# Kernel tuning notes

Measured on AMD Instinct MI355X. Metric: run time of the kernel, lower is better.

The kernel has to match this reference:

```python
import jax, jax.numpy as jnp
import numpy as np

NUM_HEADS = 16
EPS = 1e-12  # softmax_2relu eps
MASK_VALUE = -1e9  # stands in for torch.finfo(dtype).min; relu zeroes it anyway


def setup_inputs() -> dict:
    key = jax.random.key(0)
    k1, k2, k3 = jax.random.split(key, 3)
    B, S, D = 4, 1024, 1024
    hidden_states = jax.random.normal(k1, (B, S, D), dtype=jnp.float32)
    c_attn_w = jax.random.normal(k2, (D, 3 * D), dtype=jnp.float32) * 0.02
    c_attn_b = jnp.zeros((3 * D,), dtype=jnp.float32)
    c_proj_w = jax.random.normal(k3, (D, D), dtype=jnp.float32) * 0.02
    c_proj_b = jnp.zeros((D,), dtype=jnp.float32)
    return {
        "hidden_states": hidden_states,
        "c_attn_w": c_attn_w,
        "c_attn_b": c_attn_b,
        "c_proj_w": c_proj_w,
        "c_proj_b": c_proj_b,
    }


def softmax_2relu(scores, axis=-1, eps=EPS):
    r = jax.nn.relu(scores)
    n = scores.shape[axis]
    return (r + eps / n) / (jnp.sum(r, axis=axis, keepdims=True) + eps)


def reference(hidden_states, c_attn_w, c_attn_b, c_proj_w, c_proj_b):
    B, S, D = hidden_states.shape
    H = NUM_HEADS
    dh = D // H

    # fused QKV projection (Conv1D: x @ W + b)
    qkv = hidden_states @ c_attn_w + c_attn_b  # [B, S, 3D]
    q, k, v = jnp.split(qkv, 3, axis=-1)

    def to_heads(t):
        return t.reshape(B, S, H, dh).transpose(0, 2, 1, 3)  # [B, H, S, dh]

    q, k, v = to_heads(q), to_heads(k), to_heads(v)

    # attention scores, scaled
    scores = jnp.einsum("bhqd,bhkd->bhqk", q, k) / jnp.sqrt(
        jnp.asarray(dh, dtype=hidden_states.dtype)
    )

    # causal mask: masked positions set to large negative (relu -> 0)
    causal = jnp.tril(jnp.ones((S, S), dtype=bool))
    scores = jnp.where(causal[None, None, :, :], scores, MASK_VALUE)

    # custom relu-softmax normalization (softmax_2relu)
    attn = softmax_2relu(scores, axis=-1)

    ctx = jnp.einsum("bhqk,bhkd->bhqd", attn, v)  # [B, H, S, dh]
    ctx = ctx.transpose(0, 2, 1, 3).reshape(B, S, D)

    out = ctx @ c_proj_w + c_proj_b
    return out
```

## Files before the change

### kernel.cpp

```cpp
#include <hip/hip_runtime.h>
#include <hip/hip_bf16.h>

typedef unsigned short u16;
typedef unsigned int u32;

#define AS1 __attribute__((address_space(1)))
#define AS3 __attribute__((address_space(3)))

typedef __attribute__((ext_vector_type(8))) __bf16 bf16x8;
typedef __attribute__((ext_vector_type(4))) float f32x4;
typedef __attribute__((ext_vector_type(8))) u16 u16x8;

static __device__ __forceinline__ u16 f2bf(float f) {
    u32 x = __builtin_bit_cast(u32, f);
    u32 r = (x + 0x7fffu + ((x >> 16) & 1u)) >> 16;
    return (u16)r;
}
static __device__ __forceinline__ float bf2f(u16 u) {
    u32 x = ((u32)u) << 16;
    return __builtin_bit_cast(float, x);
}
static __device__ __forceinline__ void gload_lds16(const void* g, void* l) {
    __builtin_amdgcn_global_load_lds((const AS1 u32*)g, (AS3 u32*)l, 16, 0, 0);
}
static __device__ __forceinline__ u32 cvtpk(float lo, float hi) {
    u32 r;
    asm("v_cvt_pk_bf16_f32 %0, %1, %2" : "=v"(r) : "v"(lo), "v"(hi));
    return r;
}

__global__ __launch_bounds__(256) void k_cast_bf16(const float* __restrict__ in,
                                                   u16* __restrict__ out, int n8) {
    int i = blockIdx.x * 256 + threadIdx.x;
    if (i >= n8) return;
    typedef __attribute__((ext_vector_type(4))) float fx4;
    const fx4* p = (const fx4*)in;
    fx4 a = p[2 * i], b = p[2 * i + 1];
    u16x8 o;
    o[0] = f2bf(a[0]); o[1] = f2bf(a[1]); o[2] = f2bf(a[2]); o[3] = f2bf(a[3]);
    o[4] = f2bf(b[0]); o[5] = f2bf(b[1]); o[6] = f2bf(b[2]); o[7] = f2bf(b[3]);
    *(u16x8*)(out + (size_t)i * 8) = o;
}

__global__ __launch_bounds__(256) void k_wtrans(const float* __restrict__ W,
                                                u16* __restrict__ Wt, int K_, int N_) {
    __shared__ u16 T[64][65];
    int nt = blockIdx.x, kt = blockIdx.y;
    int t = threadIdx.x, c = t & 63, r0 = t >> 6;
#pragma unroll
    for (int i = 0; i < 16; i++) {
        int k = r0 + i * 4;
        T[k][c] = f2bf(W[(size_t)(kt * 64 + k) * N_ + nt * 64 + c]);
    }
    __syncthreads();
#pragma unroll
    for (int i = 0; i < 16; i++) {
        int nn = r0 + i * 4;
        Wt[(size_t)(nt * 64 + nn) * K_ + kt * 64 + c] = T[c][nn];
    }
}

template <int EPI>
__global__ __launch_bounds__(256, 2) void k_gemm(
    const u16* __restrict__ A, const u16* __restrict__ Bt,
    const float* __restrict__ bias, float* __restrict__ outf,
    u16* __restrict__ Qb, u16* __restrict__ Kb, u16* __restrict__ Vb,
    int Msz, int Nsz, int Ksz) {
    __shared__ u16 Al[128 * 64];
    __shared__ u16 Bl[128 * 64];
    int tid = threadIdx.x;
    int m0 = blockIdx.x * 128, n0 = blockIdx.y * 128;
    int w = tid >> 6, lane = tid & 63, l15 = lane & 15, lg = lane >> 4;
    int wr = (w >> 1) * 64, wc = (w & 1) * 64;
    f32x4 acc[4][4] = {};

    for (int k0 = 0; k0 < Ksz; k0 += 64) {
#pragma unroll
        for (int i = 0; i < 4; i++) {
            int c = i * 256 + tid;
            gload_lds16(A + (size_t)(m0 + (c >> 3)) * Ksz + k0 + (c & 7) * 8,
                        &Al[(c & ~63) * 8]);
        }
#pragma unroll
        for (int i = 0; i < 4; i++) {
            int c = i * 256 + tid;
            gload_lds16(Bt + (size_t)(n0 + (c >> 3)) * Ksz + k0 + (c & 7) * 8,
                        &Bl[(c & ~63) * 8]);
        }
        __syncthreads();
#pragma unroll
        for (int kk = 0; kk < 2; kk++) {
            bf16x8 af[4], bfr[4];
#pragma unroll
            for (int m = 0; m < 4; m++)
                af[m] = *(const bf16x8*)&Al[(wr + m * 16 + l15) * 64 + kk * 32 + lg * 8];
#pragma unroll
            for (int n = 0; n < 4; n++)
                bfr[n] = *(const bf16x8*)&Bl[(wc + n * 16 + l15) * 64 + kk * 32 + lg * 8];
#pragma unroll
            for (int m = 0; m < 4; m++)
#pragma unroll
                for (int n = 0; n < 4; n++)
                    acc[m][n] = __builtin_amdgcn_mfma_f32_16x16x32_bf16(af[m], bfr[n], acc[m][n], 0, 0, 0);
        }
        __syncthreads();
    }

    if (EPI == 0) {
#pragma unroll
        for (int n = 0; n < 4; n++) {
            int gn = n0 + wc + n * 16 + l15;
            float bv = bias[gn];
#pragma unroll
            for (int m = 0; m < 4; m++) {
                int gmb = m0 + wr + m * 16 + lg * 4;
#pragma unroll
                for (int r = 0; r < 4; r++)
                    outf[(size_t)(gmb + r) * Nsz + gn] = acc[m][n][r] + bv;
            }
        }
    } else {
        u16* T = Al;
        const int TP = 136;
        float bv[4];
#pragma unroll
        for (int n = 0; n < 4; n++) bv[n] = bias[n0 + wc + n * 16 + l15];
        int lrow = tid >> 3;
        int c0 = (tid & 7) << 4;
        int gcol = n0 + c0;
        int which = gcol >> 10, d = gcol & 1023, h = d >> 6, dd = d & 63;
        u16* dstb = which == 0 ? Qb : (which == 1 ? Kb : Vb);

#define EPI_CHUNK(mc)                                                              \
    {                                                                              \
        __syncthreads();                                                           \
        if (((mc) >> 1) == (w >> 1)) {                                             \
            _Pragma("unroll") for (int n = 0; n < 4; n++) {                        \
                _Pragma("unroll") for (int r = 0; r < 4; r++) {                    \
                    int lr = (lg << 2) + r;                                        \
                    T[lr * TP + wc + (n << 4) + l15] =                             \
                        f2bf(acc[2 * ((mc) & 1)][n][r] + bv[n]);                   \
                    T[(16 + lr) * TP + wc + (n << 4) + l15] =                      \
                        f2bf(acc[2 * ((mc) & 1) + 1][n][r] + bv[n]);               \
                }                                                                  \
            }                                                                      \
        }                                                                          \
        __syncthreads();                                                           \
        int gm = m0 + (mc) * 32 + lrow;                                            \
        int b = gm >> 10, s = gm & 1023;                                           \
        u16* dp = dstb + ((size_t)(b * 16 + h) * 1024 + s) * 64 + dd;              \
        const u16* sp = &T[lrow * TP + c0];                                        \
        *(u16x8*)dp = *(const u16x8*)sp;                                           \
        *(u16x8*)(dp + 8) = *(const u16x8*)(sp + 8);                               \
    }

        EPI_CHUNK(0) EPI_CHUNK(1) EPI_CHUNK(2) EPI_CHUNK(3)
#undef EPI_CHUNK
    }
}

__global__ __launch_bounds__(256) void k_vtrans(const u16* __restrict__ Vb,
                                                u16* __restrict__ Vt,
                                                float* __restrict__ vpart) {
    __shared__ u16 T[64][65];
    __shared__ float red[4][64];
    int st = blockIdx.x, bh = blockIdx.y;
    int t = threadIdx.x, c = t & 63, r0 = t >> 6;
    const u16* Vh = Vb + (size_t)bh * 65536;
    u16* Vth = Vt + (size_t)bh * 65536;
    float a = 0.f;
#pragma unroll
    for (int i = 0; i < 16; i++) {
        int s = r0 + i * 4;
        u16 v = Vh[(size_t)(st * 64 + s) * 64 + c];
        T[s][c] = v;
        a += bf2f(v);
    }
    red[r0][c] = a;
    __syncthreads();
#pragma unroll
    for (int i = 0; i < 16; i++) {
        int d = r0 + i * 4;
        Vth[(size_t)d * 1024 + st * 64 + c] = T[c][d];
    }
    if (r0 == 0)
        vpart[((size_t)bh * 16 + st) * 64 + c] =
            red[0][c] + red[1][c] + red[2][c] + red[3][c];
}

__global__ __launch_bounds__(256) void k_vsum2(const float* __restrict__ vpart,
                                               float* __restrict__ vsum) {
    int idx = blockIdx.x * 256 + threadIdx.x;
    int bh = idx >> 6, d = idx & 63;
    const float* p = vpart + (size_t)bh * 1024 + d;
    float s = 0.f;
#pragma unroll
    for (int st = 0; st < 16; st++) s += p[st * 64];
    vsum[idx] = s;
}

__global__ __launch_bounds__(512, 4) void k_attn(const u16* __restrict__ Qb,
                                                 const u16* __restrict__ Kb,
                                                 const u16* __restrict__ Vt,
                                                 const float* __restrict__ vsum,
                                                 u16* __restrict__ ctx) {
    __shared__ u16 Kl[2][4096];
    __shared__ u16 Vl[2][4096];
    __shared__ u16 Pl[8 * 1024];
    __shared__ float rsw[8][16];
    int tid = threadIdx.x, w = tid >> 6, lane = tid & 63, l15 = lane & 15, lg = lane >> 4;
    int p = blockIdx.x;
    int tb = 7 - (p >> 6);
    int bh = p & 63;
    int qb = tb * 128 + w * 16;
    int nkb = 2 * tb + 2;
    int klast = (qb + 15) >> 6;

    const u16* Qh = Qb + (size_t)bh * 65536;
    const u16* Kh = Kb + (size_t)bh * 65536;
    const u16* Vh = Vt + (size_t)bh * 65536;
    u16* Pw = &Pl[w * 1024];
    int swz = (l15 & 7) << 4;
    int q = qb + l15;

    bf16x8 qf[2];
#pragma unroll
    for (int kk = 0; kk < 2; kk++)
        qf[kk] = *(const bf16x8*)(Qh + (size_t)q * 64 + kk * 32 + lg * 8);
    float vs[4];
#pragma unroll
    for (int n = 0; n < 4; n++) vs[n] = vsum[bh * 64 + n * 16 + l15];

    int srow = tid >> 3, schunk = tid & 7;
    int soff = ((schunk * 16) ^ ((srow & 7) << 4)) >> 1;
    u16* kdst = &Kl[0][0] + w * 512;
    u16* vdst = &Vl[0][0] + w * 512;

    f32x4 ctxa[4] = {};
    float rsp = 0.f;
    int cur = 0;

    gload_lds16(Kh + (size_t)srow * 64 + soff, kdst);
    gload_lds16(Vh + (size_t)srow * 1024 + soff, vdst);
    __syncthreads();

    for (int kb = 0; kb < nkb; kb++) {
        if (kb + 1 < nkb) {
            int nx = cur ^ 1;
            gload_lds16(Kh + (size_t)(((kb + 1) << 6) + srow) * 64 + soff,
                        &Kl[nx][0] + w * 512);
            gload_lds16(Vh + (size_t)srow * 1024 + ((kb + 1) << 6) + soff,
                        &Vl[nx][0] + w * 512);
        }
        if (kb <= klast) {
            bool masked = (kb == klast);
            const char* Kc = (const char*)&Kl[cur][0];
            const char* Vc = (const char*)&Vl[cur][0];
            f32x4 sc[4] = {};
#pragma unroll
            for (int kk = 0; kk < 2; kk++)
#pragma unroll
                for (int n = 0; n < 4; n++) {
                    bf16x8 kf = *(const bf16x8*)(Kc + ((((n * 16 + l15) << 7) + (kk << 6) + (lg << 4)) ^ swz));
                    sc[n] = __builtin_amdgcn_mfma_f32_16x16x32_bf16(kf, qf[kk], sc[n], 0, 0, 0);
                }
            int qml = q - (kb << 6) - (lg << 2);
#pragma unroll
            for (int n = 0; n < 4; n++) {
                float v0 = fmaxf(sc[n][0] * 0.125f, 0.f);
                float v1 = fmaxf(sc[n][1] * 0.125f, 0.f);
                float v2 = fmaxf(sc[n][2] * 0.125f, 0.f);
                float v3 = fmaxf(sc[n][3] * 0.125f, 0.f);
                if (masked) {
                    int c = qml - n * 16;
                    v0 = (0 <= c) ? v0 : 0.f;
                    v1 = (1 <= c) ? v1 : 0.f;
                    v2 = (2 <= c) ? v2 : 0.f;
                    v3 = (3 <= c) ? v3 : 0.f;
                }
                rsp += (v0 + v1) + (v2 + v3);
                u32 w0 = cvtpk(v0, v1), w1 = cvtpk(v2, v3);
                int base = l15 * 128 + n * 32 + lg * 8;
                *(u32*)((char*)Pw + ((base) ^ swz)) = w0;
                *(u32*)((char*)Pw + ((base + 4) ^ swz)) = w1;
            }
            bf16x8 pf0 = *(const bf16x8*)((char*)Pw + ((l15 * 128 + lg * 16) ^ swz));
            bf16x8 pf1 = *(const bf16x8*)((char*)Pw + ((l15 * 128 + 64 + lg * 16) ^ swz));
#pragma unroll
            for (int n = 0; n < 4; n++) {
                bf16x8 vf = *(const bf16x8*)(Vc + ((((n * 16 + l15) << 7) + (lg << 4)) ^ swz));
                ctxa[n] = __builtin_amdgcn_mfma_f32_16x16x32_bf16(pf0, vf, ctxa[n], 0, 0, 0);
            }
#pragma unroll
            for (int n = 0; n < 4; n++) {
                bf16x8 vf = *(const bf16x8*)(Vc + ((((n * 16 + l15) << 7) + 64 + (lg << 4)) ^ swz));
                ctxa[n] = __builtin_amdgcn_mfma_f32_16x16x32_bf16(pf1, vf, ctxa[n], 0, 0, 0);
            }
        }
        __syncthreads();
        cur ^= 1;
    }

    float tsum = rsp;
    tsum += __shfl_xor(tsum, 16);
    tsum += __shfl_xor(tsum, 32);
    rsw[w][l15] = tsum;
    f32x4 rv = *(f32x4*)&rsw[w][lg * 4];
    const float EPS = 1e-12f, EPSN = 1e-12f / 1024.f;
    float inv[4];
#pragma unroll
    for (int r = 0; r < 4; r++) inv[r] = 1.f / (rv[r] + EPS);
    int b = bh >> 4, h = bh & 15;
#pragma unroll
    for (int n = 0; n < 4; n++) {
#pragma unroll
        for (int r = 0; r < 4; r++) {
            int qq = qb + lg * 4 + r;
            float val = (ctxa[n][r] + EPSN * vs[n]) * inv[r];
            ctx[(size_t)(b * 1024 + qq) * 1024 + h * 64 + n * 16 + l15] = f2bf(val);
        }
    }
}

__global__ __launch_bounds__(256) void k_qkfix(const float* __restrict__ X,
                                               const float* __restrict__ W,
                                               const float* __restrict__ bias,
                                               float* __restrict__ Qf,
                                               float* __restrict__ Kf) {
    __shared__ float red[4][8][64];
    int cb = blockIdx.x;
    int b = blockIdx.y >> 1, rh = blockIdx.y & 1;
    int tid = threadIdx.x, w = tid >> 6, lane = tid & 63;
    int col = cb * 64 + lane;

    const float* Wp = W + (size_t)(w * 256) * 3072 + col;
    const float* Xp = X + ((size_t)b * 1024 + rh * 8) * 1024 + w * 256;
    float acc[8] = {};
#pragma unroll 8
    for (int it = 0; it < 256; ++it) {
        float wv = Wp[(size_t)it * 3072];
#pragma unroll
        for (int j = 0; j < 8; j++) acc[j] += Xp[(size_t)j * 1024 + it] * wv;
    }
#pragma unroll
    for (int j = 0; j < 8; j++) red[w][j][lane] = acc[j];
    __syncthreads();

    int isK = cb >> 4, h = cb & 15;
    float* dst = isK ? Kf : Qf;
#pragma unroll
    for (int o = tid; o < 512; o += 256) {
        int j = o >> 6, c = o & 63;
        float s = red[0][j][c] + red[1][j][c] + red[2][j][c] + red[3][j][c];
        dst[((size_t)(b * 16 + h) * 16 + rh * 8 + j) * 64 + c] = s + bias[cb * 64 + c];
    }
}

__global__ __launch_bounds__(256) void k_attnfix(const float* __restrict__ Qf,
                                                 const float* __restrict__ Kf,
                                                 const u16* __restrict__ Vb,
                                                 const float* __restrict__ vsum,
                                                 u16* __restrict__ ctx) {
    __shared__ float ps[16][17];
    __shared__ float dens[16];
    int bh = blockIdx.x, t = threadIdx.x;
    int q = t >> 4, k = t & 15;
    const float* Qr = Qf + ((size_t)bh * 16 + q) * 64;
    const float* Kr = Kf + ((size_t)bh * 16 + k) * 64;
    float s = 0.f;
    for (int d = 0; d < 64; d++) s += Qr[d] * Kr[d];
    s *= 0.125f;
    float p = (k <= q) ? fmaxf(s, 0.f) : 0.f;
    float den = p;
    den += __shfl_xor(den, 1); den += __shfl_xor(den, 2);
    den += __shfl_xor(den, 4); den += __shfl_xor(den, 8);
    ps[q][k] = p;
    if (k == 0) dens[q] = den;
    __syncthreads();
    int d0 = (t & 15) * 4;
    float c[4] = {};
    for (int kk = 0; kk <= q; kk++) {
        float pv = ps[q][kk];
        const u16* vr = Vb + ((size_t)bh * 1024 + kk) * 64 + d0;
        c[0] += pv * bf2f(vr[0]); c[1] += pv * bf2f(vr[1]);
        c[2] += pv * bf2f(vr[2]); c[3] += pv * bf2f(vr[3]);
    }
    float inv = 1.f / (dens[q] + 1e-12f);
    const float EPSN = 1e-12f / 1024.f;
    const float* vs = vsum + bh * 64 + d0;
    int b = bh >> 4, h = bh & 15;
    u16* dst = ctx + (size_t)(b * 1024 + q) * 1024 + h * 64 + d0;
#pragma unroll
    for (int j = 0; j < 4; j++) dst[j] = f2bf((c[j] + EPSN * vs[j]) * inv);
}

extern "C" void kernel_launch(void* const* d_in, const int* in_sizes, int n_in,
                              void* d_out, int out_size, void* d_ws, size_t ws_size,
                              hipStream_t stream) {
    const float* X = (const float*)d_in[0];
    const float* Wqkv = (const float*)d_in[1];
    const float* bqkv = (const float*)d_in[2];
    const float* Wproj = (const float*)d_in[3];
    const float* bproj = (const float*)d_in[4];
    float* out = (float*)d_out;
    char* ws = (char*)d_ws;

    u16* Xb     = (u16*)(ws);
    u16* Wqkvt  = (u16*)(ws + 8388608);
    u16* Wprojt = (u16*)(ws + 14680064);
    u16* Qb     = (u16*)(ws + 16777216);
    u16* Kb     = (u16*)(ws + 25165824);
    u16* Vb     = (u16*)(ws + 33554432);
    u16* Vt     = (u16*)(ws + 41943040);
    float* vsum = (float*)(ws + 50331648);
    float* Qf   = (float*)(ws + 50348032);
    float* Kf   = (float*)(ws + 50610176);
    float* vpart= (float*)(ws + 50872320);
    u16* ctx    = Xb;

    k_cast_bf16<<<dim3(2048), dim3(256), 0, stream>>>(X, Xb, 524288);
    k_wtrans<<<dim3(48, 16), dim3(256), 0, stream>>>(Wqkv, Wqkvt, 1024, 3072);
    k_wtrans<<<dim3(16, 16), dim3(256), 0, stream>>>(Wproj, Wprojt, 1024, 1024);
    k_gemm<1><<<dim3(32, 24), dim3(256), 0, stream>>>(Xb, Wqkvt, bqkv, nullptr,
                                                      Qb, Kb, Vb, 4096, 3072, 1024);
    k_vtrans<<<dim3(16, 64), dim3(256), 0, stream>>>(Vb, Vt, vpart);
    k_vsum2<<<dim3(16), dim3(256), 0, stream>>>(vpart, vsum);
    k_qkfix<<<dim3(32, 8), dim3(256), 0, stream>>>(X, Wqkv, bqkv, Qf, Kf);
    k_attn<<<dim3(512), dim3(512), 0, stream>>>(Qb, Kb, Vt, vsum, ctx);
    k_attnfix<<<dim3(64), dim3(256), 0, stream>>>(Qf, Kf, Vb, vsum, ctx);
    k_gemm<0><<<dim3(32, 8), dim3(256), 0, stream>>>(ctx, Wprojt, bproj, out,
                                                     nullptr, nullptr, nullptr, 4096, 1024, 1024);
}
```

Baseline: 138.5 us.

## Fuse prep kernels, fold V transpose into QKV epilogue, retile projection GEMM

Merges the X cast and both weight transposes into one k_prep launch. The QKV GEMM epilogue now writes V directly in transposed layout and emits per-tile V column sums, which removes the separate k_vtrans pass. It still writes only the first 32 rows of V per head in row-major form, presumably for k_attnfix. The output projection moves to a dedicated 128x64-tile GEMM that launches twice as many blocks, and s_setprio hints are added around the MFMA sections of the attention kernel. The tradeoffs are fewer launches and one less global V round trip, against more complex epilogue LDS access patterns and strided Vt writes.

```diff
diff --git a/kernel.cpp b/kernel.cpp
--- a/kernel.cpp
+++ b/kernel.cpp
@@ -29,24 +29,34 @@
     return r;
 }
 
-__global__ __launch_bounds__(256) void k_cast_bf16(const float* __restrict__ in,
-                                                   u16* __restrict__ out, int n8) {
-    int i = blockIdx.x * 256 + threadIdx.x;
-    if (i >= n8) return;
-    typedef __attribute__((ext_vector_type(4))) float fx4;
-    const fx4* p = (const fx4*)in;
-    fx4 a = p[2 * i], b = p[2 * i + 1];
-    u16x8 o;
-    o[0] = f2bf(a[0]); o[1] = f2bf(a[1]); o[2] = f2bf(a[2]); o[3] = f2bf(a[3]);
-    o[4] = f2bf(b[0]); o[5] = f2bf(b[1]); o[6] = f2bf(b[2]); o[7] = f2bf(b[3]);
-    *(u16x8*)(out + (size_t)i * 8) = o;
-}
-
-__global__ __launch_bounds__(256) void k_wtrans(const float* __restrict__ W,
-                                                u16* __restrict__ Wt, int K_, int N_) {
+__global__ __launch_bounds__(256) void k_prep(const float* __restrict__ X,
+                                              u16* __restrict__ Xb,
+                                              const float* __restrict__ Wqkv,
+                                              u16* __restrict__ Wqkvt,
+                                              const float* __restrict__ Wproj,
+                                              u16* __restrict__ Wprojt) {
     __shared__ u16 T[64][65];
-    int nt = blockIdx.x, kt = blockIdx.y;
-    int t = threadIdx.x, c = t & 63, r0 = t >> 6;
+    int bid = blockIdx.x, t = threadIdx.x;
+    if (bid < 2048) {
+        int i = bid * 256 + t;
+        typedef __attribute__((ext_vector_type(4))) float fx4;
+        const fx4* p = (const fx4*)X;
+        fx4 a = p[2 * i], b = p[2 * i + 1];
+        u16x8 o;
+        o[0] = f2bf(a[0]); o[1] = f2bf(a[1]); o[2] = f2bf(a[2]); o[3] = f2bf(a[3]);
+        o[4] = f2bf(b[0]); o[5] = f2bf(b[1]); o[6] = f2bf(b[2]); o[7] = f2bf(b[3]);
+        *(u16x8*)(Xb + (size_t)i * 8) = o;
+        return;
+    }
+    const float* W; u16* Wt; int N_, nt, kt;
+    if (bid < 2816) {
+        W = Wqkv; Wt = Wqkvt; N_ = 3072;
+        int u = bid - 2048; nt = u % 48; kt = u / 48;
+    } else {
+        W = Wproj; Wt = Wprojt; N_ = 1024;
+        int u = bid - 2816; nt = u & 15; kt = u >> 4;
+    }
+    int c = t & 63, r0 = t >> 6;
 #pragma unroll
     for (int i = 0; i < 16; i++) {
         int k = r0 + i * 4;
@@ -56,7 +66,7 @@
 #pragma unroll
     for (int i = 0; i < 16; i++) {
         int nn = r0 + i * 4;
-        Wt[(size_t)(nt * 64 + nn) * K_ + kt * 64 + c] = T[c][nn];
+        Wt[(size_t)(nt * 64 + nn) * 1024 + kt * 64 + c] = T[c][nn];
     }
 }
 
@@ -65,6 +75,7 @@
     const u16* __restrict__ A, const u16* __restrict__ Bt,
     const float* __restrict__ bias, float* __restrict__ outf,
     u16* __restrict__ Qb, u16* __restrict__ Kb, u16* __restrict__ Vb,
+    u16* __restrict__ Vt, float* __restrict__ vpart,
     int Msz, int Nsz, int Ksz) {
     __shared__ u16 Al[128 * 64];
     __shared__ u16 Bl[128 * 64];
@@ -130,6 +141,11 @@
         int gcol = n0 + c0;
         int which = gcol >> 10, d = gcol & 1023, h = d >> 6, dd = d & 63;
         u16* dstb = which == 0 ? Qb : (which == 1 ? Kb : Vb);
+        bool isV = (n0 >= 2048);
+        int s0 = m0 & 1023, bq = m0 >> 10;
+        int dl = tid >> 1, sh = tid & 1;
+        int bhV = bq * 16 + ((n0 - 2048) >> 6) + (dl >> 6);
+        float vp0 = 0.f, vp1 = 0.f;
 
 #define EPI_CHUNK(mc)                                                              \
     {                                                                              \
@@ -146,46 +162,104 @@
             }                                                                      \
         }                                                                          \
         __syncthreads();                                                           \
-        int gm = m0 + (mc) * 32 + lrow;                                            \
-        int b = gm >> 10, s = gm & 1023;                                           \
-        u16* dp = dstb + ((size_t)(b * 16 + h) * 1024 + s) * 64 + dd;              \
-        const u16* sp = &T[lrow * TP + c0];                                        \
-        *(u16x8*)dp = *(const u16x8*)sp;                                           \
-        *(u16x8*)(dp + 8) = *(const u16x8*)(sp + 8);                               \
+        if (!isV) {                                                                \
+            int gm = m0 + (mc) * 32 + lrow;                                        \
+            int b = gm >> 10, s = gm & 1023;                                       \
+            u16* dp = dstb + ((size_t)(b * 16 + h) * 1024 + s) * 64 + dd;          \
+            const u16* sp = &T[lrow * TP + c0];                                    \
+            *(u16x8*)dp = *(const u16x8*)sp;                                       \
+            *(u16x8*)(dp + 8) = *(const u16x8*)(sp + 8);                           \
+        } else {                                                                   \
+            if ((mc) == 0 && s0 == 0) {                                            \
+                u16* dp = dstb + ((size_t)(bq * 16 + h) * 1024 + lrow) * 64 + dd;  \
+                const u16* sp = &T[lrow * TP + c0];                                \
+                *(u16x8*)dp = *(const u16x8*)sp;                                   \
+                *(u16x8*)(dp + 8) = *(const u16x8*)(sp + 8);                       \
+            }                                                                      \
+            float vls = 0.f;                                                       \
+            u16x8 o0, o1;                                                          \
+            _Pragma("unroll") for (int r = 0; r < 8; r++) {                        \
+                u16 v = T[((sh << 4) + r) * TP + dl];                              \
+                o0[r] = v; vls += bf2f(v);                                         \
+            }                                                                      \
+            _Pragma("unroll") for (int r = 0; r < 8; r++) {                        \
+                u16 v = T[((sh << 4) + 8 + r) * TP + dl];                          \
+                o1[r] = v; vls += bf2f(v);                                         \
+            }                                                                      \
+            vls += __shfl_xor(vls, 1);                                             \
+            if ((mc) < 2) vp0 += vls; else vp1 += vls;                             \
+            u16* vtp = Vt + (size_t)bhV * 65536 + (size_t)(dl & 63) * 1024 +       \
+                       s0 + (mc) * 32 + (sh << 4);                                 \
+            *(u16x8*)vtp = o0;                                                     \
+            *(u16x8*)(vtp + 8) = o1;                                               \
+        }                                                                          \
     }
 
         EPI_CHUNK(0) EPI_CHUNK(1) EPI_CHUNK(2) EPI_CHUNK(3)
 #undef EPI_CHUNK
-    }
-}
-
-__global__ __launch_bounds__(256) void k_vtrans(const u16* __restrict__ Vb,
-                                                u16* __restrict__ Vt,
-                                                float* __restrict__ vpart) {
-    __shared__ u16 T[64][65];
-    __shared__ float red[4][64];
-    int st = blockIdx.x, bh = blockIdx.y;
-    int t = threadIdx.x, c = t & 63, r0 = t >> 6;
-    const u16* Vh = Vb + (size_t)bh * 65536;
-    u16* Vth = Vt + (size_t)bh * 65536;
-    float a = 0.f;
-#pragma unroll
-    for (int i = 0; i < 16; i++) {
-        int s = r0 + i * 4;
-        u16 v = Vh[(size_t)(st * 64 + s) * 64 + c];
-        T[s][c] = v;
-        a += bf2f(v);
-    }
-    red[r0][c] = a;
-    __syncthreads();
-#pragma unroll
-    for (int i = 0; i < 16; i++) {
-        int d = r0 + i * 4;
-        Vth[(size_t)d * 1024 + st * 64 + c] = T[c][d];
-    }
-    if (r0 == 0)
-        vpart[((size_t)bh * 16 + st) * 64 + c] =
-            red[0][c] + red[1][c] + red[2][c] + red[3][c];
+
+        if (isV && sh == 0) {
+            int st0 = s0 >> 6;
+            vpart[((size_t)bhV * 16 + st0) * 64 + (dl & 63)] = vp0;
+            vpart[((size_t)bhV * 16 + st0 + 1) * 64 + (dl & 63)] = vp1;
+        }
+    }
+}
+
+__global__ __launch_bounds__(256, 2) void k_gemmP(
+    const u16* __restrict__ A, const u16* __restrict__ Bt,
+    const float* __restrict__ bias, float* __restrict__ outf) {
+    __shared__ u16 Al[128 * 64];
+    __shared__ u16 Bl[64 * 64];
+    int tid = threadIdx.x;
+    int m0 = blockIdx.x * 128, n0 = blockIdx.y * 64;
+    int w = tid >> 6, lane = tid & 63, l15 = lane & 15, lg = lane >> 4;
+    int wr = (w >> 1) * 64, wc = (w & 1) * 32;
+    f32x4 acc[4][2] = {};
+
+    for (int k0 = 0; k0 < 1024; k0 += 64) {
+#pragma unroll
+        for (int i = 0; i < 4; i++) {
+            int c = i * 256 + tid;
+            gload_lds16(A + (size_t)(m0 + (c >> 3)) * 1024 + k0 + (c & 7) * 8,
+                        &Al[(c & ~63) * 8]);
+        }
+#pragma unroll
+        for (int i = 0; i < 2; i++) {
+            int c = i * 256 + tid;
+            gload_lds16(Bt + (size_t)(n0 + (c >> 3)) * 1024 + k0 + (c & 7) * 8,
+                        &Bl[(c & ~63) * 8]);
+        }
+        __syncthreads();
+#pragma unroll
+        for (int kk = 0; kk < 2; kk++) {
+            bf16x8 af[4], bfr[2];
+#pragma unroll
+            for (int m = 0; m < 4; m++)
+                af[m] = *(const bf16x8*)&Al[(wr + m * 16 + l15) * 64 + kk * 32 + lg * 8];
+#pragma unroll
+            for (int n = 0; n < 2; n++)
+                bfr[n] = *(const bf16x8*)&Bl[(wc + n * 16 + l15) * 64 + kk * 32 + lg * 8];
+#pragma unroll
+            for (int m = 0; m < 4; m++)
+#pragma unroll
+                for (int n = 0; n < 2; n++)
+                    acc[m][n] = __builtin_amdgcn_mfma_f32_16x16x32_bf16(af[m], bfr[n], acc[m][n], 0, 0, 0);
+        }
+        __syncthreads();
+    }
+#pragma unroll
+    for (int n = 0; n < 2; n++) {
+        int gn = n0 + wc + n * 16 + l15;
+        float bv = bias[gn];
+#pragma unroll
+        for (int m = 0; m < 4; m++) {
+            int gmb = m0 + wr + m * 16 + lg * 4;
+#pragma unroll
+            for (int r = 0; r < 4; r++)
+                outf[(size_t)(gmb + r) * 1024 + gn] = acc[m][n][r] + bv;
+        }
+    }
 }
 
 __global__ __launch_bounds__(256) void k_vsum2(const float* __restrict__ vpart,
@@ -257,6 +331,7 @@
             const char* Kc = (const char*)&Kl[cur][0];
             const char* Vc = (const char*)&Vl[cur][0];
             f32x4 sc[4] = {};
+            __builtin_amdgcn_s_setprio(1);
 #pragma unroll
             for (int kk = 0; kk < 2; kk++)
 #pragma unroll
@@ -264,6 +339,7 @@
                     bf16x8 kf = *(const bf16x8*)(Kc + ((((n * 16 + l15) << 7) + (kk << 6) + (lg << 4)) ^ swz));
                     sc[n] = __builtin_amdgcn_mfma_f32_16x16x32_bf16(kf, qf[kk], sc[n], 0, 0, 0);
                 }
+            __builtin_amdgcn_s_setprio(0);
             int qml = q - (kb << 6) - (lg << 2);
 #pragma unroll
             for (int n = 0; n < 4; n++) {
@@ -286,6 +362,7 @@
             }
             bf16x8 pf0 = *(const bf16x8*)((char*)Pw + ((l15 * 128 + lg * 16) ^ swz));
             bf16x8 pf1 = *(const bf16x8*)((char*)Pw + ((l15 * 128 + 64 + lg * 16) ^ swz));
+            __builtin_amdgcn_s_setprio(1);
 #pragma unroll
             for (int n = 0; n < 4; n++) {
                 bf16x8 vf = *(const bf16x8*)(Vc + ((((n * 16 + l15) << 7) + (lg << 4)) ^ swz));
@@ -296,6 +373,7 @@
                 bf16x8 vf = *(const bf16x8*)(Vc + ((((n * 16 + l15) << 7) + 64 + (lg << 4)) ^ swz));
                 ctxa[n] = __builtin_amdgcn_mfma_f32_16x16x32_bf16(pf1, vf, ctxa[n], 0, 0, 0);
             }
+            __builtin_amdgcn_s_setprio(0);
         }
         __syncthreads();
         cur ^= 1;
@@ -418,16 +496,13 @@
     float* vpart= (float*)(ws + 50872320);
     u16* ctx    = Xb;
 
-    k_cast_bf16<<<dim3(2048), dim3(256), 0, stream>>>(X, Xb, 524288);
-    k_wtrans<<<dim3(48, 16), dim3(256), 0, stream>>>(Wqkv, Wqkvt, 1024, 3072);
-    k_wtrans<<<dim3(16, 16), dim3(256), 0, stream>>>(Wproj, Wprojt, 1024, 1024);
+    k_prep<<<dim3(3072), dim3(256), 0, stream>>>(X, Xb, Wqkv, Wqkvt, Wproj, Wprojt);
     k_gemm<1><<<dim3(32, 24), dim3(256), 0, stream>>>(Xb, Wqkvt, bqkv, nullptr,
-                                                      Qb, Kb, Vb, 4096, 3072, 1024);
-    k_vtrans<<<dim3(16, 64), dim3(256), 0, stream>>>(Vb, Vt, vpart);
+                                                      Qb, Kb, Vb, Vt, vpart,
+                                                      4096, 3072, 1024);
     k_vsum2<<<dim3(16), dim3(256), 0, stream>>>(vpart, vsum);
     k_qkfix<<<dim3(32, 8), dim3(256), 0, stream>>>(X, Wqkv, bqkv, Qf, Kf);
     k_attn<<<dim3(512), dim3(512), 0, stream>>>(Qb, Kb, Vt, vsum, ctx);
     k_attnfix<<<dim3(64), dim3(256), 0, stream>>>(Qf, Kf, Vb, vsum, ctx);
-    k_gemm<0><<<dim3(32, 8), dim3(256), 0, stream>>>(ctx, Wprojt, bproj, out,
-                                                     nullptr, nullptr, nullptr, 4096, 1024, 1024);
-}
+    k_gemmP<<<dim3(32, 16), dim3(256), 0, stream>>>(ctx, Wprojt, bproj, out);
+}
```

New measurement: 127.2 us. 8.2% less time.
